# Performance work log

Measured on AMD Instinct MI355X. Metric: run time of the kernel, lower is better.

The kernel has to match this reference:

```python
import jax, jax.numpy as jnp
import numpy as np

N_ITEMS = 200000
N_USER_TABLE = 262144
N_USERS = 16384
N_HIST = 819200
TEXT_DIM = 128
GCN_DIM = 128
HIDDEN_DIM = 256
TOWER_DIM = 128
EPS = 1e-12


def setup_inputs() -> dict:
    key = jax.random.key(0)
    ks = jax.random.split(key, 14)
    s = 0.02
    return {
        "item_text_emb": jax.random.normal(ks[0], (N_ITEMS, TEXT_DIM), jnp.float32),
        "gcn_item_emb": jax.random.normal(ks[1], (N_ITEMS, GCN_DIM), jnp.float32),
        "gcn_user_emb": jax.random.normal(ks[2], (N_USER_TABLE, GCN_DIM), jnp.float32),
        "w1_item": jax.random.normal(ks[3], (TEXT_DIM + GCN_DIM, HIDDEN_DIM), jnp.float32) * s,
        "b1_item": jax.random.normal(ks[4], (HIDDEN_DIM,), jnp.float32) * s,
        "w2_item": jax.random.normal(ks[5], (HIDDEN_DIM, TOWER_DIM), jnp.float32) * s,
        "b2_item": jax.random.normal(ks[6], (TOWER_DIM,), jnp.float32) * s,
        "w1_user": jax.random.normal(ks[7], (GCN_DIM + TOWER_DIM, HIDDEN_DIM), jnp.float32) * s,
        "b1_user": jax.random.normal(ks[8], (HIDDEN_DIM,), jnp.float32) * s,
        "w2_user": jax.random.normal(ks[9], (HIDDEN_DIM, TOWER_DIM), jnp.float32) * s,
        "b2_user": jax.random.normal(ks[10], (TOWER_DIM,), jnp.float32) * s,
        "users": jax.random.randint(ks[11], (N_USERS,), 0, N_USER_TABLE, jnp.int64),
        "hist_items": jax.random.randint(ks[12], (N_HIST,), 0, N_ITEMS, jnp.int64),
        "hist_segids": jnp.sort(jax.random.randint(ks[13], (N_HIST,), 0, N_USERS, jnp.int64)),
    }


def _l2norm(x):
    # F.normalize(x, dim=1): x / max(||x||, eps)
    n = jnp.sqrt(jnp.sum(x * x, axis=1, keepdims=True))
    return x / jnp.maximum(n, EPS)


def reference(item_text_emb, gcn_item_emb, gcn_user_emb,
              w1_item, b1_item, w2_item, b2_item,
              w1_user, b1_user, w2_user, b2_user,
              users, hist_items, hist_segids):
    # encode_items: MLP over [text || gcn] then L2 normalize
    xi = jnp.concatenate([item_text_emb, gcn_item_emb], axis=1)  # [N_ITEMS, 256]
    hi = jax.nn.relu(xi @ w1_item + b1_item)
    item_emb = _l2norm(hi @ w2_item + b2_item)  # [N_ITEMS, TOWER_DIM]

    # ragged per-user history mean pooling (segment mean over sorted segment ids)
    gathered = item_emb[hist_items]  # [N_HIST, TOWER_DIM]
    sums = jax.ops.segment_sum(gathered, hist_segids, num_segments=N_USERS,
                               indices_are_sorted=True)
    counts = jax.ops.segment_sum(jnp.ones((hist_segids.shape[0],), item_emb.dtype),
                                 hist_segids, num_segments=N_USERS,
                                 indices_are_sorted=True)
    # users with empty history -> zeros(TOWER_DIM)
    hist = jnp.where(counts[:, None] > 0, sums / jnp.maximum(counts[:, None], 1.0), 0.0)

    xu = jnp.concatenate([gcn_user_emb[users], hist], axis=1)  # [N_USERS, 256]
    hu = jax.nn.relu(xu @ w1_user + b1_user)
    user_emb = _l2norm(hu @ w2_user + b2_user)  # [N_USERS, TOWER_DIM]
    return user_emb, item_emb
```

## Files before the change

### kernel.cpp

```cpp
#include <hip/hip_runtime.h>
#include <stdint.h>

#define N_ITEMS   200000
#define N_USERS   16384
#define N_HIST    819200

typedef short bfrag8 __attribute__((ext_vector_type(8)));
typedef float ffrag4 __attribute__((ext_vector_type(4)));

__device__ __forceinline__ unsigned short f2bf(float f) {
    union { float f; unsigned int u; } v; v.f = f;
    unsigned int u = v.u;
    u += 0x7fffu + ((u >> 16) & 1u);
    return (unsigned short)(u >> 16);
}

__device__ __forceinline__ ffrag4 mfma16(bfrag8 a, bfrag8 b, ffrag4 c) {
    return __builtin_amdgcn_mfma_f32_16x16x32_bf16(a, b, c, 0, 0, 0);
}

__global__ void cvtT_kernel(const float* __restrict__ w, unsigned short* __restrict__ o,
                            int K, int N) {
    int id = blockIdx.x * 256 + threadIdx.x;
    if (id >= K * N) return;
    int n = id / K;
    int k = id - n * K;
    o[id] = f2bf(w[(size_t)k * N + n]);
}

#define BM 64
#define A_STRIDE 528
#define W_STRIDE 80
#define A_BYTES  (BM * A_STRIDE)
#define W_BYTES  (256 * W_STRIDE)

__global__ __launch_bounds__(256) void tower_kernel(
    const float* __restrict__ srcA, const float* __restrict__ srcB,
    const int* __restrict__ rowIdxA,
    const unsigned short* __restrict__ w1t, const float* __restrict__ b1,
    const unsigned short* __restrict__ w2t, const float* __restrict__ b2,
    float* __restrict__ out)
{
    __shared__ __align__(16) char smem[A_BYTES + W_BYTES];
    char* smemA = smem;
    char* smemW = smem + A_BYTES;

    const int rowsBase = blockIdx.x * BM;
    const int lane = threadIdx.x & 63;
    const int wave = threadIdx.x >> 6;
    const int lr = lane & 15;
    const int lg = lane >> 4;
    const int R0 = wave * 16;

    for (int i = 0; i < 8; ++i) {
        int c  = threadIdx.x + 256 * i;
        int r  = c >> 5;
        int cb = c & 31;
        int gr = rowsBase + r;
        const float* src;
        if (cb < 16) {
            int sr = rowIdxA ? rowIdxA[gr] : gr;
            src = srcA + (size_t)sr * 128 + cb * 8;
        } else {
            src = srcB + (size_t)gr * 128 + (cb - 16) * 8;
        }
        float4 x0 = ((const float4*)src)[0];
        float4 x1 = ((const float4*)src)[1];
        uint4 w;
        w.x = (unsigned)f2bf(x0.x) | ((unsigned)f2bf(x0.y) << 16);
        w.y = (unsigned)f2bf(x0.z) | ((unsigned)f2bf(x0.w) << 16);
        w.z = (unsigned)f2bf(x1.x) | ((unsigned)f2bf(x1.y) << 16);
        w.w = (unsigned)f2bf(x1.z) | ((unsigned)f2bf(x1.w) << 16);
        *(uint4*)(smemA + r * A_STRIDE + cb * 16) = w;
    }

    ffrag4 acc[16];
#pragma unroll
    for (int i = 0; i < 16; ++i) acc[i] = (ffrag4){0.f, 0.f, 0.f, 0.f};

    for (int kt = 0; kt < 8; ++kt) {
        __syncthreads();
        {
            int n = threadIdx.x;
            const uint4* g = (const uint4*)((const char*)w1t + (size_t)n * 512 + kt * 64);
            uint4* d = (uint4*)(smemW + n * W_STRIDE);
            d[0] = g[0]; d[1] = g[1]; d[2] = g[2]; d[3] = g[3];
        }
        __syncthreads();
        bfrag8 a = *(const bfrag8*)(smemA + (R0 + lr) * A_STRIDE + kt * 64 + lg * 16);
#pragma unroll
        for (int nt = 0; nt < 16; ++nt) {
            bfrag8 b = *(const bfrag8*)(smemW + (nt * 16 + lr) * W_STRIDE + lg * 16);
            acc[nt] = mfma16(a, b, acc[nt]);
        }
    }

#pragma unroll
    for (int nt = 0; nt < 16; ++nt) {
        int col = nt * 16 + lr;
        float bias = b1[col];
#pragma unroll
        for (int r = 0; r < 4; ++r) {
            float v = acc[nt][r] + bias;
            v = fmaxf(v, 0.f);
            int row = R0 + lg * 4 + r;
            *(unsigned short*)(smemA + row * A_STRIDE + col * 2) = f2bf(v);
        }
    }

    ffrag4 acc2[8];
#pragma unroll
    for (int i = 0; i < 8; ++i) acc2[i] = (ffrag4){0.f, 0.f, 0.f, 0.f};

    for (int kt = 0; kt < 8; ++kt) {
        __syncthreads();
        if (threadIdx.x < 128) {
            int n = threadIdx.x;
            const uint4* g = (const uint4*)((const char*)w2t + (size_t)n * 512 + kt * 64);
            uint4* d = (uint4*)(smemW + n * W_STRIDE);
            d[0] = g[0]; d[1] = g[1]; d[2] = g[2]; d[3] = g[3];
        }
        __syncthreads();
        bfrag8 a = *(const bfrag8*)(smemA + (R0 + lr) * A_STRIDE + kt * 64 + lg * 16);
#pragma unroll
        for (int nt = 0; nt < 8; ++nt) {
            bfrag8 b = *(const bfrag8*)(smemW + (nt * 16 + lr) * W_STRIDE + lg * 16);
            acc2[nt] = mfma16(a, b, acc2[nt]);
        }
    }

    float y[8][4];
    float p0 = 0.f, p1 = 0.f, p2 = 0.f, p3 = 0.f;
#pragma unroll
    for (int nt = 0; nt < 8; ++nt) {
        int col = nt * 16 + lr;
        float bias = b2[col];
        float v;
        v = acc2[nt][0] + bias; y[nt][0] = v; p0 += v * v;
        v = acc2[nt][1] + bias; y[nt][1] = v; p1 += v * v;
        v = acc2[nt][2] + bias; y[nt][2] = v; p2 += v * v;
        v = acc2[nt][3] + bias; y[nt][3] = v; p3 += v * v;
    }
#pragma unroll
    for (int off = 8; off >= 1; off >>= 1) {
        p0 += __shfl_xor(p0, off, 16);
        p1 += __shfl_xor(p1, off, 16);
        p2 += __shfl_xor(p2, off, 16);
        p3 += __shfl_xor(p3, off, 16);
    }
    float s0 = 1.f / fmaxf(sqrtf(p0), 1e-12f);
    float s1 = 1.f / fmaxf(sqrtf(p1), 1e-12f);
    float s2 = 1.f / fmaxf(sqrtf(p2), 1e-12f);
    float s3 = 1.f / fmaxf(sqrtf(p3), 1e-12f);
#pragma unroll
    for (int nt = 0; nt < 8; ++nt) {
        int col = nt * 16 + lr;
        size_t rb = (size_t)(rowsBase + R0 + lg * 4) * 128 + col;
        out[rb + 0 * 128] = y[nt][0] * s0;
        out[rb + 1 * 128] = y[nt][1] * s1;
        out[rb + 2 * 128] = y[nt][2] * s2;
        out[rb + 3 * 128] = y[nt][3] * s3;
    }
}

__global__ __launch_bounds__(64) void pool_kernel(
    const float* __restrict__ itemEmb,
    const int* __restrict__ histItems,
    const int* __restrict__ histSeg,
    float* __restrict__ hist)
{
    const int u = blockIdx.x;
    const int lane = threadIdx.x;

    int lo = 0, hi = N_HIST;
    while (lo < hi) { int m = (lo + hi) >> 1; if (histSeg[m] < u) lo = m + 1; else hi = m; }
    const int s = lo;
    hi = N_HIST;
    while (lo < hi) { int m = (lo + hi) >> 1; if (histSeg[m] < u + 1) lo = m + 1; else hi = m; }
    const int e = lo;

    float ax = 0.f, ay = 0.f;
    for (int i = s; i < e; ++i) {
        int idx = histItems[i];
        float2 v = *(const float2*)(itemEmb + (size_t)idx * 128 + lane * 2);
        ax += v.x; ay += v.y;
    }
    int cnt = e - s;
    float inv = (cnt > 0) ? 1.f / (float)cnt : 0.f;
    float2 r; r.x = ax * inv; r.y = ay * inv;
    *(float2*)(hist + (size_t)u * 128 + lane * 2) = r;
}

extern "C" void kernel_launch(void* const* d_in, const int* in_sizes, int n_in,
                              void* d_out, int out_size, void* d_ws, size_t ws_size,
                              hipStream_t stream) {
    const float* text    = (const float*)d_in[0];
    const float* gcnItem = (const float*)d_in[1];
    const float* gcnUser = (const float*)d_in[2];
    const float* w1i = (const float*)d_in[3];
    const float* b1i = (const float*)d_in[4];
    const float* w2i = (const float*)d_in[5];
    const float* b2i = (const float*)d_in[6];
    const float* w1u = (const float*)d_in[7];
    const float* b1u = (const float*)d_in[8];
    const float* w2u = (const float*)d_in[9];
    const float* b2u = (const float*)d_in[10];
    const int* users     = (const int*)d_in[11];
    const int* histItems = (const int*)d_in[12];
    const int* histSeg   = (const int*)d_in[13];

    float* outUser = (float*)d_out;
    float* outItem = (float*)d_out + (size_t)N_USERS * 128;

    char* ws = (char*)d_ws;
    unsigned short* w1ti = (unsigned short*)(ws + 0);
    unsigned short* w2ti = (unsigned short*)(ws + 131072);
    unsigned short* w1tu = (unsigned short*)(ws + 196608);
    unsigned short* w2tu = (unsigned short*)(ws + 327680);
    float*          hist = (float*)(ws + 393216);

    cvtT_kernel<<<256, 256, 0, stream>>>(w1i, w1ti, 256, 256);
    cvtT_kernel<<<128, 256, 0, stream>>>(w2i, w2ti, 256, 128);
    cvtT_kernel<<<256, 256, 0, stream>>>(w1u, w1tu, 256, 256);
    cvtT_kernel<<<128, 256, 0, stream>>>(w2u, w2tu, 256, 128);

    tower_kernel<<<N_ITEMS / BM, 256, 0, stream>>>(
        text, gcnItem, nullptr, w1ti, b1i, w2ti, b2i, outItem);

    pool_kernel<<<N_USERS, 64, 0, stream>>>(outItem, histItems, histSeg, hist);

    tower_kernel<<<N_USERS / BM, 256, 0, stream>>>(
        gcnUser, hist, users, w1tu, b1u, w2tu, b2u, outUser);
}
```

Baseline: 325.1 us.

## Persistent tower kernel with resident W1, register W2, prefetch, and bf16 pooling mirror

Replaces the per-tile tower kernel with a persistent kernel. It keeps all of W1 in swizzled LDS and W2 fragments in registers, and prefetches the next 32-row tile's inputs into registers while computing the current one. Pooling now gathers a bf16 mirror of the item embeddings written by the item tower, which halves gather bytes, and runs four users per block. The four weight conversions are merged into one launch. The bf16 mirror adds rounding to the pooled history, and using it depends on workspace size.

```diff
diff --git a/kernel.cpp b/kernel.cpp
--- a/kernel.cpp
+++ b/kernel.cpp
@@ -19,158 +19,222 @@
     return __builtin_amdgcn_mfma_f32_16x16x32_bf16(a, b, c, 0, 0, 0);
 }
 
-__global__ void cvtT_kernel(const float* __restrict__ w, unsigned short* __restrict__ o,
-                            int K, int N) {
+__device__ __forceinline__ bfrag8 pack8(float4 x0, float4 x1) {
+    bfrag8 o;
+    o[0] = (short)f2bf(x0.x); o[1] = (short)f2bf(x0.y);
+    o[2] = (short)f2bf(x0.z); o[3] = (short)f2bf(x0.w);
+    o[4] = (short)f2bf(x1.x); o[5] = (short)f2bf(x1.y);
+    o[6] = (short)f2bf(x1.z); o[7] = (short)f2bf(x1.w);
+    return o;
+}
+
+__global__ void cvt_all_kernel(const float* __restrict__ w1i, const float* __restrict__ w2i,
+                               const float* __restrict__ w1u, const float* __restrict__ w2u,
+                               unsigned short* __restrict__ o1i, unsigned short* __restrict__ o2i,
+                               unsigned short* __restrict__ o1u, unsigned short* __restrict__ o2u) {
     int id = blockIdx.x * 256 + threadIdx.x;
-    if (id >= K * N) return;
-    int n = id / K;
-    int k = id - n * K;
-    o[id] = f2bf(w[(size_t)k * N + n]);
-}
-
-#define BM 64
-#define A_STRIDE 528
-#define W_STRIDE 80
-#define A_BYTES  (BM * A_STRIDE)
-#define W_BYTES  (256 * W_STRIDE)
-
-__global__ __launch_bounds__(256) void tower_kernel(
+    const float* w; unsigned short* o; int N; int local;
+    if (id < 65536)       { w = w1i; o = o1i; N = 256; local = id; }
+    else if (id < 98304)  { w = w2i; o = o2i; N = 128; local = id - 65536; }
+    else if (id < 163840) { w = w1u; o = o1u; N = 256; local = id - 98304; }
+    else                  { w = w2u; o = o2u; N = 128; local = id - 163840; }
+    int n = local >> 8;
+    int k = local & 255;
+    o[local] = f2bf(w[(size_t)k * N + n]);
+}
+
+#define LOAD_A(tt)  do { \
+    int rb_ = (tt) * 32; \
+    _Pragma("unroll") \
+    for (int mi_ = 0; mi_ < 2; ++mi_) { \
+        int r_ = rb_ + mi_ * 16 + lr; \
+        int ra_ = rowIdxA ? rowIdxA[r_] : r_; \
+        const float* pA_ = srcA + (size_t)ra_ * 128; \
+        const float* pB_ = srcB + (size_t)r_ * 128; \
+        _Pragma("unroll") \
+        for (int kt_ = 0; kt_ < 8; ++kt_) { \
+            const float* p_ = (kt_ < 4) ? (pA_ + kt_ * 32 + lg * 8) \
+                                        : (pB_ + (kt_ - 4) * 32 + lg * 8); \
+            a4[mi_][kt_][0] = ((const float4*)p_)[0]; \
+            a4[mi_][kt_][1] = ((const float4*)p_)[1]; \
+        } \
+    } } while (0)
+
+__global__ __launch_bounds__(256, 1) void tower2_kernel(
     const float* __restrict__ srcA, const float* __restrict__ srcB,
     const int* __restrict__ rowIdxA,
     const unsigned short* __restrict__ w1t, const float* __restrict__ b1,
     const unsigned short* __restrict__ w2t, const float* __restrict__ b2,
-    float* __restrict__ out)
+    float* __restrict__ out, unsigned short* __restrict__ mirror,
+    int nTiles)
 {
-    __shared__ __align__(16) char smem[A_BYTES + W_BYTES];
-    char* smemA = smem;
-    char* smemW = smem + A_BYTES;
-
-    const int rowsBase = blockIdx.x * BM;
-    const int lane = threadIdx.x & 63;
-    const int wave = threadIdx.x >> 6;
-    const int lr = lane & 15;
-    const int lg = lane >> 4;
-    const int R0 = wave * 16;
-
-    for (int i = 0; i < 8; ++i) {
-        int c  = threadIdx.x + 256 * i;
-        int r  = c >> 5;
-        int cb = c & 31;
-        int gr = rowsBase + r;
-        const float* src;
-        if (cb < 16) {
-            int sr = rowIdxA ? rowIdxA[gr] : gr;
-            src = srcA + (size_t)sr * 128 + cb * 8;
-        } else {
-            src = srcB + (size_t)gr * 128 + (cb - 16) * 8;
-        }
-        float4 x0 = ((const float4*)src)[0];
-        float4 x1 = ((const float4*)src)[1];
-        uint4 w;
-        w.x = (unsigned)f2bf(x0.x) | ((unsigned)f2bf(x0.y) << 16);
-        w.y = (unsigned)f2bf(x0.z) | ((unsigned)f2bf(x0.w) << 16);
-        w.z = (unsigned)f2bf(x1.x) | ((unsigned)f2bf(x1.y) << 16);
-        w.w = (unsigned)f2bf(x1.z) | ((unsigned)f2bf(x1.w) << 16);
-        *(uint4*)(smemA + r * A_STRIDE + cb * 16) = w;
+    __shared__ __align__(16) char smem[131072 + 16384];
+    char* sW1 = smem;
+    char* sH  = smem + 131072;
+    float* sPn = (float*)(smem + 131072);
+
+    const int tid  = threadIdx.x;
+    const int lane = tid & 63;
+    const int wav  = tid >> 6;
+    const int lr   = lane & 15;
+    const int lg   = lane >> 4;
+
+    {
+        const uint4* g = (const uint4*)w1t;
+#pragma unroll
+        for (int i = 0; i < 32; ++i) {
+            int c = tid + 256 * i;
+            int n = c >> 5, k16 = c & 31;
+            uint4 v = g[c];
+            *(uint4*)(sW1 + n * 512 + ((k16 * 16) ^ ((n & 7) << 4))) = v;
+        }
     }
 
-    ffrag4 acc[16];
-#pragma unroll
-    for (int i = 0; i < 16; ++i) acc[i] = (ffrag4){0.f, 0.f, 0.f, 0.f};
-
-    for (int kt = 0; kt < 8; ++kt) {
+    bfrag8 w2f[2][8];
+#pragma unroll
+    for (int j = 0; j < 2; ++j) {
+        int n2 = wav * 32 + j * 16 + lr;
+#pragma unroll
+        for (int kt = 0; kt < 8; ++kt)
+            w2f[j][kt] = *(const bfrag8*)((const char*)w2t + (size_t)n2 * 512 + kt * 64 + lg * 16);
+    }
+    float b1v[4];
+#pragma unroll
+    for (int i = 0; i < 4; ++i) b1v[i] = b1[(wav * 4 + i) * 16 + lr];
+    float b2v[2];
+#pragma unroll
+    for (int j = 0; j < 2; ++j) b2v[j] = b2[wav * 32 + j * 16 + lr];
+
+    __syncthreads();
+
+    const int stride = (int)gridDim.x;
+    int t = (int)blockIdx.x;
+    float4 a4[2][8][2];
+    if (t < nTiles) LOAD_A(t);
+
+    for (; t < nTiles; t += stride) {
+        bfrag8 af[2][8];
+#pragma unroll
+        for (int mi = 0; mi < 2; ++mi)
+#pragma unroll
+            for (int kt = 0; kt < 8; ++kt)
+                af[mi][kt] = pack8(a4[mi][kt][0], a4[mi][kt][1]);
+        int tn = t + stride;
+        if (tn < nTiles) LOAD_A(tn);
+
+        ffrag4 acc[2][4];
+#pragma unroll
+        for (int mi = 0; mi < 2; ++mi)
+#pragma unroll
+            for (int i = 0; i < 4; ++i) acc[mi][i] = (ffrag4){0.f, 0.f, 0.f, 0.f};
+#pragma unroll
+        for (int kt = 0; kt < 8; ++kt) {
+#pragma unroll
+            for (int i = 0; i < 4; ++i) {
+                int n = (wav * 4 + i) * 16 + lr;
+                bfrag8 b = *(const bfrag8*)(sW1 + n * 512 + ((kt * 64 + lg * 16) ^ ((n & 7) << 4)));
+                acc[0][i] = mfma16(af[0][kt], b, acc[0][i]);
+                acc[1][i] = mfma16(af[1][kt], b, acc[1][i]);
+            }
+        }
+
+#pragma unroll
+        for (int i = 0; i < 4; ++i) {
+            int col = (wav * 4 + i) * 16 + lr;
+#pragma unroll
+            for (int mi = 0; mi < 2; ++mi)
+#pragma unroll
+                for (int r = 0; r < 4; ++r) {
+                    float v = fmaxf(acc[mi][i][r] + b1v[i], 0.f);
+                    int row = mi * 16 + lg * 4 + r;
+                    *(unsigned short*)(sH + row * 512 + ((col * 2) ^ ((row & 7) << 4))) = f2bf(v);
+                }
+        }
         __syncthreads();
-        {
-            int n = threadIdx.x;
-            const uint4* g = (const uint4*)((const char*)w1t + (size_t)n * 512 + kt * 64);
-            uint4* d = (uint4*)(smemW + n * W_STRIDE);
-            d[0] = g[0]; d[1] = g[1]; d[2] = g[2]; d[3] = g[3];
-        }
+
+        ffrag4 acc2[2][2];
+#pragma unroll
+        for (int m = 0; m < 2; ++m)
+#pragma unroll
+            for (int j = 0; j < 2; ++j) acc2[m][j] = (ffrag4){0.f, 0.f, 0.f, 0.f};
+#pragma unroll
+        for (int kt = 0; kt < 8; ++kt) {
+#pragma unroll
+            for (int m = 0; m < 2; ++m) {
+                int row = m * 16 + lr;
+                bfrag8 ha = *(const bfrag8*)(sH + row * 512 + ((kt * 64 + lg * 16) ^ ((row & 7) << 4)));
+                acc2[m][0] = mfma16(ha, w2f[0][kt], acc2[m][0]);
+                acc2[m][1] = mfma16(ha, w2f[1][kt], acc2[m][1]);
+            }
+        }
+
+        float y[2][2][4];
+        float pn[2][4];
+#pragma unroll
+        for (int m = 0; m < 2; ++m)
+#pragma unroll
+            for (int r = 0; r < 4; ++r) pn[m][r] = 0.f;
+#pragma unroll
+        for (int m = 0; m < 2; ++m)
+#pragma unroll
+            for (int j = 0; j < 2; ++j)
+#pragma unroll
+                for (int r = 0; r < 4; ++r) {
+                    float v = acc2[m][j][r] + b2v[j];
+                    y[m][j][r] = v;
+                    pn[m][r] += v * v;
+                }
+#pragma unroll
+        for (int m = 0; m < 2; ++m)
+#pragma unroll
+            for (int r = 0; r < 4; ++r) {
+                float s = pn[m][r];
+                s += __shfl_xor(s, 1, 16);
+                s += __shfl_xor(s, 2, 16);
+                s += __shfl_xor(s, 4, 16);
+                s += __shfl_xor(s, 8, 16);
+                pn[m][r] = s;
+            }
         __syncthreads();
-        bfrag8 a = *(const bfrag8*)(smemA + (R0 + lr) * A_STRIDE + kt * 64 + lg * 16);
-#pragma unroll
-        for (int nt = 0; nt < 16; ++nt) {
-            bfrag8 b = *(const bfrag8*)(smemW + (nt * 16 + lr) * W_STRIDE + lg * 16);
-            acc[nt] = mfma16(a, b, acc[nt]);
-        }
+        if (lr == 0) {
+#pragma unroll
+            for (int m = 0; m < 2; ++m)
+#pragma unroll
+                for (int r = 0; r < 4; ++r)
+                    sPn[(m * 16 + lg * 4 + r) * 4 + wav] = pn[m][r];
+        }
+        __syncthreads();
+
+        int rb = t * 32;
+#pragma unroll
+        for (int m = 0; m < 2; ++m)
+#pragma unroll
+            for (int r = 0; r < 4; ++r) {
+                float4 q = *(float4*)(sPn + (m * 16 + lg * 4 + r) * 4);
+                float s = q.x + q.y + q.z + q.w;
+                float sc = 1.f / fmaxf(sqrtf(s), 1e-12f);
+                int row = rb + m * 16 + lg * 4 + r;
+#pragma unroll
+                for (int j = 0; j < 2; ++j) {
+                    int col = wav * 32 + j * 16 + lr;
+                    float v = y[m][j][r] * sc;
+                    out[(size_t)row * 128 + col] = v;
+                    if (mirror) mirror[(size_t)row * 128 + col] = f2bf(v);
+                }
+            }
+        __syncthreads();
     }
-
-#pragma unroll
-    for (int nt = 0; nt < 16; ++nt) {
-        int col = nt * 16 + lr;
-        float bias = b1[col];
-#pragma unroll
-        for (int r = 0; r < 4; ++r) {
-            float v = acc[nt][r] + bias;
-            v = fmaxf(v, 0.f);
-            int row = R0 + lg * 4 + r;
-            *(unsigned short*)(smemA + row * A_STRIDE + col * 2) = f2bf(v);
-        }
-    }
-
-    ffrag4 acc2[8];
-#pragma unroll
-    for (int i = 0; i < 8; ++i) acc2[i] = (ffrag4){0.f, 0.f, 0.f, 0.f};
-
-    for (int kt = 0; kt < 8; ++kt) {
-        __syncthreads();
-        if (threadIdx.x < 128) {
-            int n = threadIdx.x;
-            const uint4* g = (const uint4*)((const char*)w2t + (size_t)n * 512 + kt * 64);
-            uint4* d = (uint4*)(smemW + n * W_STRIDE);
-            d[0] = g[0]; d[1] = g[1]; d[2] = g[2]; d[3] = g[3];
-        }
-        __syncthreads();
-        bfrag8 a = *(const bfrag8*)(smemA + (R0 + lr) * A_STRIDE + kt * 64 + lg * 16);
-#pragma unroll
-        for (int nt = 0; nt < 8; ++nt) {
-            bfrag8 b = *(const bfrag8*)(smemW + (nt * 16 + lr) * W_STRIDE + lg * 16);
-            acc2[nt] = mfma16(a, b, acc2[nt]);
-        }
-    }
-
-    float y[8][4];
-    float p0 = 0.f, p1 = 0.f, p2 = 0.f, p3 = 0.f;
-#pragma unroll
-    for (int nt = 0; nt < 8; ++nt) {
-        int col = nt * 16 + lr;
-        float bias = b2[col];
-        float v;
-        v = acc2[nt][0] + bias; y[nt][0] = v; p0 += v * v;
-        v = acc2[nt][1] + bias; y[nt][1] = v; p1 += v * v;
-        v = acc2[nt][2] + bias; y[nt][2] = v; p2 += v * v;
-        v = acc2[nt][3] + bias; y[nt][3] = v; p3 += v * v;
-    }
-#pragma unroll
-    for (int off = 8; off >= 1; off >>= 1) {
-        p0 += __shfl_xor(p0, off, 16);
-        p1 += __shfl_xor(p1, off, 16);
-        p2 += __shfl_xor(p2, off, 16);
-        p3 += __shfl_xor(p3, off, 16);
-    }
-    float s0 = 1.f / fmaxf(sqrtf(p0), 1e-12f);
-    float s1 = 1.f / fmaxf(sqrtf(p1), 1e-12f);
-    float s2 = 1.f / fmaxf(sqrtf(p2), 1e-12f);
-    float s3 = 1.f / fmaxf(sqrtf(p3), 1e-12f);
-#pragma unroll
-    for (int nt = 0; nt < 8; ++nt) {
-        int col = nt * 16 + lr;
-        size_t rb = (size_t)(rowsBase + R0 + lg * 4) * 128 + col;
-        out[rb + 0 * 128] = y[nt][0] * s0;
-        out[rb + 1 * 128] = y[nt][1] * s1;
-        out[rb + 2 * 128] = y[nt][2] * s2;
-        out[rb + 3 * 128] = y[nt][3] * s3;
-    }
-}
-
-__global__ __launch_bounds__(64) void pool_kernel(
-    const float* __restrict__ itemEmb,
+}
+
+__global__ __launch_bounds__(256) void pool2_kernel(
+    const unsigned short* __restrict__ mirror,
+    const float* __restrict__ itemF,
     const int* __restrict__ histItems,
     const int* __restrict__ histSeg,
     float* __restrict__ hist)
 {
-    const int u = blockIdx.x;
-    const int lane = threadIdx.x;
+    const int u = blockIdx.x * 4 + (threadIdx.x >> 6);
+    const int lane = threadIdx.x & 63;
 
     int lo = 0, hi = N_HIST;
     while (lo < hi) { int m = (lo + hi) >> 1; if (histSeg[m] < u) lo = m + 1; else hi = m; }
@@ -180,13 +244,22 @@
     const int e = lo;
 
     float ax = 0.f, ay = 0.f;
-    for (int i = s; i < e; ++i) {
-        int idx = histItems[i];
-        float2 v = *(const float2*)(itemEmb + (size_t)idx * 128 + lane * 2);
-        ax += v.x; ay += v.y;
+    if (mirror) {
+        for (int i = s; i < e; ++i) {
+            int idx = histItems[i];
+            unsigned v = *(const unsigned*)(mirror + (size_t)idx * 128 + lane * 2);
+            union { unsigned u; float f; } c0, c1;
+            c0.u = v << 16; c1.u = v & 0xffff0000u;
+            ax += c0.f; ay += c1.f;
+        }
+    } else {
+        for (int i = s; i < e; ++i) {
+            int idx = histItems[i];
+            float2 v = *(const float2*)(itemF + (size_t)idx * 128 + lane * 2);
+            ax += v.x; ay += v.y;
+        }
     }
-    int cnt = e - s;
-    float inv = (cnt > 0) ? 1.f / (float)cnt : 0.f;
+    float inv = (e > s) ? 1.f / (float)(e - s) : 0.f;
     float2 r; r.x = ax * inv; r.y = ay * inv;
     *(float2*)(hist + (size_t)u * 128 + lane * 2) = r;
 }
@@ -218,17 +291,17 @@
     unsigned short* w1tu = (unsigned short*)(ws + 196608);
     unsigned short* w2tu = (unsigned short*)(ws + 327680);
     float*          hist = (float*)(ws + 393216);
-
-    cvtT_kernel<<<256, 256, 0, stream>>>(w1i, w1ti, 256, 256);
-    cvtT_kernel<<<128, 256, 0, stream>>>(w2i, w2ti, 256, 128);
-    cvtT_kernel<<<256, 256, 0, stream>>>(w1u, w1tu, 256, 256);
-    cvtT_kernel<<<128, 256, 0, stream>>>(w2u, w2tu, 256, 128);
-
-    tower_kernel<<<N_ITEMS / BM, 256, 0, stream>>>(
-        text, gcnItem, nullptr, w1ti, b1i, w2ti, b2i, outItem);
-
-    pool_kernel<<<N_USERS, 64, 0, stream>>>(outItem, histItems, histSeg, hist);
-
-    tower_kernel<<<N_USERS / BM, 256, 0, stream>>>(
-        gcnUser, hist, users, w1tu, b1u, w2tu, b2u, outUser);
-}
+    const size_t mirrorOff = 8781824;
+    const size_t needBytes = mirrorOff + (size_t)N_ITEMS * 128 * 2;
+    unsigned short* mirror = (ws_size >= needBytes) ? (unsigned short*)(ws + mirrorOff) : nullptr;
+
+    cvt_all_kernel<<<768, 256, 0, stream>>>(w1i, w2i, w1u, w2u, w1ti, w2ti, w1tu, w2tu);
+
+    tower2_kernel<<<512, 256, 0, stream>>>(
+        text, gcnItem, nullptr, w1ti, b1i, w2ti, b2i, outItem, mirror, N_ITEMS / 32);
+
+    pool2_kernel<<<N_USERS / 4, 256, 0, stream>>>(mirror, outItem, histItems, histSeg, hist);
+
+    tower2_kernel<<<512, 256, 0, stream>>>(
+        gcnUser, hist, users, w1tu, b1u, w2tu, b2u, outUser, nullptr, N_USERS / 32);
+}
```

Result: slower. 347.2 us (+6.8%).
